# Kernel tuning notes

Measured on AMD Instinct MI355X. Metric: run time of the kernel, lower is better.

## Reference

```python
import jax, jax.numpy as jnp
import numpy as np

IN, HID, RANK, B = 2048, 2048, 512, 8192


def setup_inputs() -> dict:
    key = jax.random.key(0)
    ks = jax.random.split(key, 16)
    s_in = 1.0 / np.sqrt(IN + HID)
    s_r = 1.0 / np.sqrt(RANK)
    inp = {
        "x": jax.random.normal(ks[0], (B, IN), jnp.float32),
        "h": jax.random.normal(ks[1], (B, HID), jnp.float32),
        "c": jax.random.normal(ks[2], (B, HID), jnp.float32),
    }
    names = ["i", "f", "c", "o"]
    for idx, g in enumerate(names):
        inp[f"U{g}"] = jax.random.uniform(ks[3 + 3 * idx], (IN + HID, RANK), jnp.float32, -s_in, s_in)
        inp[f"V{g}"] = jax.random.uniform(ks[4 + 3 * idx], (RANK, HID), jnp.float32, -s_r, s_r)
        inp[f"b{g}"] = jnp.zeros((HID,), jnp.float32)
    return inp


def reference(x, h, c, Ui, Vi, bi, Uf, Vf, bf, Uc, Vc, bc, Uo, Vo, bo):
    combined = jnp.concatenate([x, h], axis=1)  # [B, IN+HID]

    def gate(U, V, b):
        return (combined @ U) @ V + b  # low-rank: [B,R] then [B,HID]

    i = jax.nn.sigmoid(gate(Ui, Vi, bi))
    f = jax.nn.sigmoid(gate(Uf, Vf, bf))
    o = jax.nn.sigmoid(gate(Uo, Vo, bo))
    c_hat = jnp.tanh(gate(Uc, Vc, bc))
    c_new = f * c + i * c_hat
    h_new = o * jnp.tanh(c_new)
    return (h_new, c_new)
```

## Files before the change

### kernel.cpp

```cpp
#include <hip/hip_runtime.h>
#include <hip/hip_bf16.h>
#include <cstdint>
#include <cstddef>

typedef __bf16 bf16;
typedef __bf16 bf16x8 __attribute__((ext_vector_type(8)));
typedef float f32x4 __attribute__((ext_vector_type(4)));

#define BATCH 8192
#define IN_DIM 2048
#define HID 2048
#define RANK 512
#define KDIM 4096
#define NG 2048
#define CHUNK_ROWS 4096


__device__ __forceinline__ void gload16(const void* g, void* l) {
  __builtin_amdgcn_global_load_lds(
      (const __attribute__((address_space(1))) unsigned int*)g,
      (__attribute__((address_space(3))) unsigned int*)l, 16, 0, 0);
}

__device__ __forceinline__ float sigmoidf_(float x) {
  return 1.0f / (1.0f + __expf(-x));
}
__device__ __forceinline__ float tanhf_(float x) {
  return 1.0f - 2.0f / (__expf(2.0f * x) + 1.0f);
}

#define GBAR  __builtin_amdgcn_s_barrier()
#define VMC4  asm volatile("s_waitcnt vmcnt(4)" ::: "memory")
#define VMC8  asm volatile("s_waitcnt vmcnt(8)" ::: "memory")
#define SB0   __builtin_amdgcn_sched_barrier(0)
#define LGKMC(N) do { asm volatile("s_waitcnt lgkmcnt(" #N ")" ::: "memory"); SB0; } while (0)

__device__ __forceinline__ void stage_half(const bf16* __restrict__ g0, int ld,
                                           int row0, int kcol, bf16* lbase, int tid) {
  const int wid = tid >> 6;
  #pragma unroll
  for (int q = 0; q < 2; ++q) {
    const int slot = q * 512 + tid;
    const int row = slot >> 3, cb = slot & 7;
    const int gcb = cb ^ (row & 7);
    gload16(g0 + (size_t)(row0 + row) * ld + kcol + gcb * 8,
            lbase + (size_t)(q * 64 + wid * 8) * 64);
  }
}

#define LD_APAR(PA, Q, P)                                                      \
  _Pragma("unroll") for (int ai = 0; ai < 2; ++ai)                             \
  _Pragma("unroll") for (int ks = 0; ks < 2; ++ks)                             \
    a[P][ai][ks] = *(const bf16x8*)((PA) + (wm + (Q) * 32 + ai * 16 + lr) * 64 \
                                 + ((((ks << 2) | lk) ^ sw) << 3));

#define LD_Bp(PB)                                                              \
  _Pragma("unroll") for (int j = 0; j < 4; ++j)                                \
  _Pragma("unroll") for (int ks = 0; ks < 2; ++ks)                             \
    b[j][ks] = *(const bf16x8*)((PB) + (wn + j * 16 + lr) * 64                 \
                                 + ((((ks << 2) | lk) ^ sw) << 3));

#define MFMAQP(Q, P)                                                           \
  _Pragma("unroll") for (int ai = 0; ai < 2; ++ai)                             \
  _Pragma("unroll") for (int ks = 0; ks < 2; ++ks)                             \
  _Pragma("unroll") for (int j = 0; j < 4; ++j)                                \
    acc[(Q) * 2 + ai][j] = __builtin_amdgcn_mfma_f32_16x16x32_bf16(            \
        a[P][ai][ks], b[j][ks], acc[(Q) * 2 + ai][j], 0, 0, 0);


template <int NT>
__device__ __forceinline__ void gemm_core(const bf16* __restrict__ A, int lda, int m0,
                                          const bf16* __restrict__ B, int ldb, int n0,
                                          bf16* lds, f32x4 (&acc)[8][4]) {
  const int tid = threadIdx.x;
  const int wid = tid >> 6, lane = tid & 63;
  const int wm = (wid >> 2) * 128, wn = (wid & 3) * 64;
  const int lr = lane & 15, lk = lane >> 4;
  const int sw = lr & 7;
  bf16x8 a[2][2][2];
  bf16x8 b[4][2];

  bf16* Ab0 = lds;
  bf16* Ab1 = lds + 16384;
  bf16* Rg0 = lds + 2 * 16384;
  bf16* Rg1 = lds + 3 * 16384;
  bf16* Rg2 = lds + 4 * 16384;

  #pragma unroll
  for (int i = 0; i < 8; ++i)
    #pragma unroll
    for (int j = 0; j < 4; ++j) acc[i][j] = (f32x4){0.f, 0.f, 0.f, 0.f};

  stage_half(A, lda, m0,       0,   Ab0,        tid);
  stage_half(A, lda, m0 + 128, 0,   Ab0 + 8192, tid);
  stage_half(B, ldb, n0,       0,   Rg0,        tid);
  stage_half(B, ldb, n0 + 128, 0,   Rg0 + 8192, tid);
  stage_half(B, ldb, n0,       64,  Rg1,        tid);
  stage_half(B, ldb, n0 + 128, 64,  Rg1 + 8192, tid);
  stage_half(B, ldb, n0,       128, Rg2,        tid);
  stage_half(B, ldb, n0 + 128, 128, Rg2 + 8192, tid);
  VMC8;
  GBAR;
  LD_Bp(Rg0);
  SB0;

  bf16 *pBc = Rg0, *pBn = Rg1, *pBn2 = Rg2;
  bf16 *pAc = Ab0, *pAa = Ab1;
  for (int c = 0; c < NT; ++c) {
    const int kc1 = ((c + 1) & (NT - 1)) * 64;
    const int kc3 = ((c + 3) & (NT - 1)) * 64;
    LD_APAR(pAc, 0, 0); LD_APAR(pAc, 1, 1); SB0;
    stage_half(A, lda, m0,       kc1, pAa,        tid); SB0;
    GBAR;
    LGKMC(4);
    __builtin_amdgcn_s_setprio(1); MFMAQP(0, 0); __builtin_amdgcn_s_setprio(0);
    LD_APAR(pAc, 2, 0); SB0;
    stage_half(A, lda, m0 + 128, kc1, pAa + 8192, tid); SB0;
    GBAR;
    LGKMC(4);
    __builtin_amdgcn_s_setprio(1); MFMAQP(1, 1); __builtin_amdgcn_s_setprio(0);
    LD_APAR(pAc, 3, 1); SB0;
    stage_half(B, ldb, n0,       kc3, pBc,        tid); SB0;
    GBAR;
    LGKMC(4);
    __builtin_amdgcn_s_setprio(1); MFMAQP(2, 0); __builtin_amdgcn_s_setprio(0);
    stage_half(B, ldb, n0 + 128, kc3, pBc + 8192, tid); SB0;
    VMC4;
    GBAR;
    LGKMC(0);
    __builtin_amdgcn_s_setprio(1); MFMAQP(3, 1); __builtin_amdgcn_s_setprio(0);
    LD_Bp(pBn);
    SB0;
    bf16* tt = pBc; pBc = pBn; pBn = pBn2; pBn2 = tt;
    tt = pAc; pAc = pAa; pAa = tt;
  }
}


__global__ void k_convert_combined(const float* __restrict__ x,
                                   const float* __restrict__ h,
                                   bf16* __restrict__ out) {
  size_t i4 = (size_t)blockIdx.x * blockDim.x + threadIdx.x;
  size_t base = i4 * 4;
  int col = (int)(base & (KDIM - 1));
  size_t row = base >> 12;
  const float* src = (col < IN_DIM) ? (x + row * IN_DIM + col)
                                    : (h + row * (size_t)HID + (col - IN_DIM));
  float4 v = *(const float4*)src;
  union { bf16 b[4]; uint2 u; } p;
  p.b[0] = (bf16)v.x; p.b[1] = (bf16)v.y; p.b[2] = (bf16)v.z; p.b[3] = (bf16)v.w;
  *(uint2*)(out + base) = p.u;
}


__global__ void k_tconv4(const float* __restrict__ s0, const float* __restrict__ s1,
                         const float* __restrict__ s2, const float* __restrict__ s3,
                         bf16* __restrict__ out, int nrow, int ncol,
                         long ostride, long gstride) {
  __shared__ float t[32][33];
  const float* in = blockIdx.z == 0 ? s0 : blockIdx.z == 1 ? s1
                  : blockIdx.z == 2 ? s2 : s3;
  bf16* o = out + (size_t)blockIdx.z * gstride;
  int c0 = blockIdx.x * 32, r0 = blockIdx.y * 32;
  int tx = threadIdx.x, ty = threadIdx.y;
  #pragma unroll
  for (int yy = ty; yy < 32; yy += 8)
    t[yy][tx] = in[(size_t)(r0 + yy) * ncol + c0 + tx];
  __syncthreads();
  #pragma unroll
  for (int yy = ty; yy < 32; yy += 8)
    o[(size_t)(c0 + yy) * ostride + r0 + tx] = (bf16)t[tx][yy];
}


__launch_bounds__(512, 2)
__global__ void k_gemm1(const bf16* __restrict__ A,
                        const bf16* __restrict__ Bt,
                        bf16* __restrict__ R) {
  __shared__ __align__(16) bf16 lds[81920];
  const int bx = blockIdx.x;
  const int id = (bx & 7) * 32 + (bx >> 3);
  const int m0 = (id >> 3) * 256, n0 = (id & 7) * 256;
  f32x4 acc[8][4];
  gemm_core<KDIM / 64>(A, KDIM, m0, Bt, KDIM, n0, lds, acc);

  const int tid = threadIdx.x;
  const int wid = tid >> 6, lane = tid & 63;
  const int wm = (wid >> 2) * 128, wn = (wid & 3) * 64;
  const int lr = lane & 15, lk = lane >> 4;
  #pragma unroll
  for (int i = 0; i < 8; ++i)
    #pragma unroll
    for (int j = 0; j < 4; ++j)
      #pragma unroll
      for (int v = 0; v < 4; ++v)
        R[(size_t)(m0 + wm + i * 16 + lk * 4 + v) * NG + (n0 + wn + j * 16 + lr)] =
            (bf16)acc[i][j][v];
}


__launch_bounds__(512, 2)
__global__ void k_gates(const bf16* __restrict__ Rb,
                        const bf16* __restrict__ Vt,
                        const float* __restrict__ b0, const float* __restrict__ b1,
                        const float* __restrict__ b2, const float* __restrict__ b3,
                        bf16* __restrict__ G, int m_base) {
  __shared__ __align__(16) bf16 lds[81920];
  const int bx = blockIdx.x;
  const int id = (bx & 7) * 64 + (bx >> 3);
  const int gate = id >> 7;
  const int mo = ((id >> 3) & 15) * 256;
  const int n0 = (id & 7) * 256;
  f32x4 acc[8][4];
  gemm_core<RANK / 64>(Rb + gate * RANK, NG, m_base + mo,
                       Vt + (size_t)gate * HID * RANK, RANK, n0, lds, acc);

  const int tid = threadIdx.x;
  const int wid = tid >> 6, lane = tid & 63;
  const int wm = (wid >> 2) * 128, wn = (wid & 3) * 64;
  const int lr = lane & 15, lk = lane >> 4;
  const float* bias = gate == 0 ? b0 : gate == 1 ? b1 : gate == 2 ? b2 : b3;
  const bool is_tanh = (gate == 2);
  bf16* Gg = G + (size_t)gate * CHUNK_ROWS * HID;
  #pragma unroll
  for (int j = 0; j < 4; ++j) {
    const int col = n0 + wn + j * 16 + lr;
    const float bj = bias[col];
    #pragma unroll
    for (int i = 0; i < 8; ++i)
      #pragma unroll
      for (int v = 0; v < 4; ++v) {
        const int row = mo + wm + i * 16 + lk * 4 + v;
        float p = acc[i][j][v] + bj;
        float av = is_tanh ? tanhf_(p) : sigmoidf_(p);
        Gg[(size_t)row * HID + col] = (bf16)av;
      }
  }
}


__global__ void k_ew(const bf16* __restrict__ G,
                     const float* __restrict__ cin,
                     float* __restrict__ hout, float* __restrict__ cout,
                     int m_base) {
  const size_t CHUNK = (size_t)CHUNK_ROWS * HID;
  const bf16* Gi = G;
  const bf16* Gf = G + CHUNK;
  const bf16* Gc = G + 2 * CHUNK;
  const bf16* Go = G + 3 * CHUNK;
  const size_t n8 = CHUNK / 8;
  for (size_t t = (size_t)blockIdx.x * blockDim.x + threadIdx.x; t < n8;
       t += (size_t)gridDim.x * blockDim.x) {
    size_t e = t * 8;
    bf16x8 vi = *(const bf16x8*)(Gi + e);
    bf16x8 vf = *(const bf16x8*)(Gf + e);
    bf16x8 vc = *(const bf16x8*)(Gc + e);
    bf16x8 vo = *(const bf16x8*)(Go + e);
    size_t ge = (size_t)m_base * HID + e;
    float4 c0 = *(const float4*)(cin + ge);
    float4 c1 = *(const float4*)(cin + ge + 4);
    float cc[8] = {c0.x, c0.y, c0.z, c0.w, c1.x, c1.y, c1.z, c1.w};
    float cn[8], hn[8];
    #pragma unroll
    for (int v = 0; v < 8; ++v) {
      float iv = (float)vi[v], fv = (float)vf[v], cv = (float)vc[v], ov = (float)vo[v];
      cn[v] = fv * cc[v] + iv * cv;
      hn[v] = ov * tanhf_(cn[v]);
    }
    *(float4*)(cout + ge)     = (float4){cn[0], cn[1], cn[2], cn[3]};
    *(float4*)(cout + ge + 4) = (float4){cn[4], cn[5], cn[6], cn[7]};
    *(float4*)(hout + ge)     = (float4){hn[0], hn[1], hn[2], hn[3]};
    *(float4*)(hout + ge + 4) = (float4){hn[4], hn[5], hn[6], hn[7]};
  }
}


extern "C" void kernel_launch(void* const* d_in, const int* in_sizes, int n_in,
                              void* d_out, int out_size, void* d_ws, size_t ws_size,
                              hipStream_t stream) {
  const float* x = (const float*)d_in[0];
  const float* h = (const float*)d_in[1];
  const float* c = (const float*)d_in[2];
  const float* U[4] = {(const float*)d_in[3], (const float*)d_in[6],
                       (const float*)d_in[9], (const float*)d_in[12]};
  const float* V[4] = {(const float*)d_in[4], (const float*)d_in[7],
                       (const float*)d_in[10], (const float*)d_in[13]};
  const float* b[4] = {(const float*)d_in[5], (const float*)d_in[8],
                       (const float*)d_in[11], (const float*)d_in[14]};

  char* ws = (char*)d_ws;
  bf16* combined = (bf16*)ws;
  bf16* Ut       = (bf16*)(ws + 67108864);
  bf16* Vt       = (bf16*)(ws + 67108864 + 16777216);
  bf16* Rbuf     = (bf16*)(ws + 67108864 + 16777216 + 8388608);
  bf16* G        = (bf16*)ws;

  float* hout = (float*)d_out;
  float* cout = hout + (size_t)BATCH * HID;

  k_convert_combined<<<(BATCH * (size_t)KDIM / 4) / 256, 256, 0, stream>>>(x, h, combined);

  k_tconv4<<<dim3(RANK / 32, KDIM / 32, 4), dim3(32, 8), 0, stream>>>(
      U[0], U[1], U[2], U[3], Ut, KDIM, RANK, KDIM, (long)RANK * KDIM);
  k_tconv4<<<dim3(HID / 32, RANK / 32, 4), dim3(32, 8), 0, stream>>>(
      V[0], V[1], V[2], V[3], Vt, RANK, HID, RANK, (long)HID * RANK);

  k_gemm1<<<256, 512, 0, stream>>>(combined, Ut, Rbuf);

  for (int chunk = 0; chunk < 2; ++chunk) {
    int m_base = chunk * CHUNK_ROWS;
    k_gates<<<512, 512, 0, stream>>>(Rbuf, Vt, b[0], b[1], b[2], b[3], G, m_base);
    k_ew<<<2048, 256, 0, stream>>>(G, c, hout, cout, m_base);
  }
}
```

Measured before the change: 343.6 us.

## Fuse gate GEMMs pairwise with elementwise LSTM cell update epilogues

Replaces the per-chunk gate GEMM plus separate elementwise kernel with two kernels. Each computes two gates' second-stage GEMMs on a 256x128 tile: the first writes sigmoid(i)*tanh(c_hat) as bf16, the second computes f and o and finishes c_new and h_new in its epilogue. This removes the four bf16 gate buffers and their round trip through memory. In exchange it uses a new smaller-tile GEMM core with a different wait schedule, holds two accumulator sets per thread (more register pressure), and the final epilogue does scalar, less coalesced fp32 loads and stores.

```diff
diff --git a/kernel.cpp b/kernel.cpp
--- a/kernel.cpp
+++ b/kernel.cpp
@@ -13,7 +13,6 @@
 #define RANK 512
 #define KDIM 4096
 #define NG 2048
-#define CHUNK_ROWS 4096
 
 
 __device__ __forceinline__ void gload16(const void* g, void* l) {
@@ -30,6 +29,8 @@
 }
 
 #define GBAR  __builtin_amdgcn_s_barrier()
+#define VMC0  asm volatile("s_waitcnt vmcnt(0)" ::: "memory")
+#define VMC2  asm volatile("s_waitcnt vmcnt(2)" ::: "memory")
 #define VMC4  asm volatile("s_waitcnt vmcnt(4)" ::: "memory")
 #define VMC8  asm volatile("s_waitcnt vmcnt(8)" ::: "memory")
 #define SB0   __builtin_amdgcn_sched_barrier(0)
@@ -48,16 +49,17 @@
   }
 }
 
+#define LD_Bp(PB)                                                              \
+  _Pragma("unroll") for (int j = 0; j < 4; ++j)                                \
+  _Pragma("unroll") for (int ks = 0; ks < 2; ++ks)                             \
+    b[j][ks] = *(const bf16x8*)((PB) + (wn + j * 16 + lr) * 64                 \
+                                 + ((((ks << 2) | lk) ^ sw) << 3));
+
+
 #define LD_APAR(PA, Q, P)                                                      \
   _Pragma("unroll") for (int ai = 0; ai < 2; ++ai)                             \
   _Pragma("unroll") for (int ks = 0; ks < 2; ++ks)                             \
     a[P][ai][ks] = *(const bf16x8*)((PA) + (wm + (Q) * 32 + ai * 16 + lr) * 64 \
-                                 + ((((ks << 2) | lk) ^ sw) << 3));
-
-#define LD_Bp(PB)                                                              \
-  _Pragma("unroll") for (int j = 0; j < 4; ++j)                                \
-  _Pragma("unroll") for (int ks = 0; ks < 2; ++ks)                             \
-    b[j][ks] = *(const bf16x8*)((PB) + (wn + j * 16 + lr) * 64                 \
                                  + ((((ks << 2) | lk) ^ sw) << 3));
 
 #define MFMAQP(Q, P)                                                           \
@@ -66,7 +68,6 @@
   _Pragma("unroll") for (int j = 0; j < 4; ++j)                                \
     acc[(Q) * 2 + ai][j] = __builtin_amdgcn_mfma_f32_16x16x32_bf16(            \
         a[P][ai][ks], b[j][ks], acc[(Q) * 2 + ai][j], 0, 0, 0);
-
 
 template <int NT>
 __device__ __forceinline__ void gemm_core(const bf16* __restrict__ A, int lda, int m0,
@@ -129,6 +130,81 @@
     GBAR;
     LGKMC(0);
     __builtin_amdgcn_s_setprio(1); MFMAQP(3, 1); __builtin_amdgcn_s_setprio(0);
+    LD_Bp(pBn);
+    SB0;
+    bf16* tt = pBc; pBc = pBn; pBn = pBn2; pBn2 = tt;
+    tt = pAc; pAc = pAa; pAa = tt;
+  }
+}
+
+
+#define LD_AP(PA, Q, P)                                                        \
+  _Pragma("unroll") for (int ks = 0; ks < 2; ++ks)                             \
+    ap[P][ks] = *(const bf16x8*)((PA) + (wm + (Q) * 16 + lr) * 64              \
+                                 + ((((ks << 2) | lk) ^ sw) << 3));
+
+#define MFMAP(Q, P)                                                            \
+  _Pragma("unroll") for (int ks = 0; ks < 2; ++ks)                             \
+  _Pragma("unroll") for (int j = 0; j < 4; ++j)                                \
+    acc[(Q)][j] = __builtin_amdgcn_mfma_f32_16x16x32_bf16(                     \
+        ap[P][ks], b[j][ks], acc[(Q)][j], 0, 0, 0);
+
+template <int NT>
+__device__ __forceinline__ void gemm_coreP(const bf16* __restrict__ A, int lda, int m0,
+                                           const bf16* __restrict__ B, int ldb, int n0,
+                                           bf16* lds, f32x4 (&acc)[4][4]) {
+  const int tid = threadIdx.x;
+  const int wid = tid >> 6, lane = tid & 63;
+  const int wm = (wid >> 1) * 64, wn = (wid & 1) * 64;
+  const int lr = lane & 15, lk = lane >> 4;
+  const int sw = lr & 7;
+  bf16x8 ap[2][2], b[4][2];
+
+  bf16* Ab0 = lds;
+  bf16* Ab1 = lds + 16384;
+  bf16* Rg0 = lds + 32768;
+  bf16* Rg1 = lds + 40960;
+  bf16* Rg2 = lds + 49152;
+
+  #pragma unroll
+  for (int i = 0; i < 4; ++i)
+    #pragma unroll
+    for (int j = 0; j < 4; ++j) acc[i][j] = (f32x4){0.f, 0.f, 0.f, 0.f};
+
+  stage_half(A, lda, m0,       0,   Ab0,        tid);
+  stage_half(A, lda, m0 + 128, 0,   Ab0 + 8192, tid);
+  stage_half(B, ldb, n0, 0,   Rg0, tid);
+  stage_half(B, ldb, n0, 64,  Rg1, tid);
+  stage_half(B, ldb, n0, 128, Rg2, tid);
+  VMC4;
+  GBAR;
+  LD_Bp(Rg0);
+  SB0;
+
+  bf16 *pBc = Rg0, *pBn = Rg1, *pBn2 = Rg2;
+  bf16 *pAc = Ab0, *pAa = Ab1;
+  for (int c = 0; c < NT; ++c) {
+    const int kc1 = ((c + 1) & (NT - 1)) * 64;
+    const int kc3 = ((c + 3) & (NT - 1)) * 64;
+    LD_AP(pAc, 0, 0); LD_AP(pAc, 1, 1); SB0;
+    stage_half(A, lda, m0,       kc1, pAa,        tid); SB0;
+    GBAR;
+    LGKMC(2);
+    __builtin_amdgcn_s_setprio(1); MFMAP(0, 0); __builtin_amdgcn_s_setprio(0);
+    LD_AP(pAc, 2, 0); SB0;
+    stage_half(A, lda, m0 + 128, kc1, pAa + 8192, tid); SB0;
+    GBAR;
+    LGKMC(2);
+    __builtin_amdgcn_s_setprio(1); MFMAP(1, 1); __builtin_amdgcn_s_setprio(0);
+    LD_AP(pAc, 3, 1); SB0;
+    stage_half(B, ldb, n0, kc3, pBc, tid); SB0;
+    GBAR;
+    LGKMC(2);
+    __builtin_amdgcn_s_setprio(1); MFMAP(2, 0); __builtin_amdgcn_s_setprio(0);
+    VMC2;
+    LGKMC(0);
+    GBAR;
+    __builtin_amdgcn_s_setprio(1); MFMAP(3, 1); __builtin_amdgcn_s_setprio(0);
     LD_Bp(pBn);
     SB0;
     bf16* tt = pBc; pBc = pBn; pBn = pBn2; pBn2 = tt;
@@ -200,77 +276,82 @@
 
 
 __launch_bounds__(512, 2)
-__global__ void k_gates(const bf16* __restrict__ Rb,
-                        const bf16* __restrict__ Vt,
-                        const float* __restrict__ b0, const float* __restrict__ b1,
-                        const float* __restrict__ b2, const float* __restrict__ b3,
-                        bf16* __restrict__ G, int m_base) {
-  __shared__ __align__(16) bf16 lds[81920];
+__global__ void k_pair_ic(const bf16* __restrict__ Rb,
+                          const bf16* __restrict__ Vt,
+                          const float* __restrict__ bi, const float* __restrict__ bc,
+                          bf16* __restrict__ sv) {
+  __shared__ __align__(16) bf16 lds[57344];
   const int bx = blockIdx.x;
   const int id = (bx & 7) * 64 + (bx >> 3);
-  const int gate = id >> 7;
-  const int mo = ((id >> 3) & 15) * 256;
-  const int n0 = (id & 7) * 256;
-  f32x4 acc[8][4];
-  gemm_core<RANK / 64>(Rb + gate * RANK, NG, m_base + mo,
-                       Vt + (size_t)gate * HID * RANK, RANK, n0, lds, acc);
-
-  const int tid = threadIdx.x;
-  const int wid = tid >> 6, lane = tid & 63;
-  const int wm = (wid >> 2) * 128, wn = (wid & 3) * 64;
-  const int lr = lane & 15, lk = lane >> 4;
-  const float* bias = gate == 0 ? b0 : gate == 1 ? b1 : gate == 2 ? b2 : b3;
-  const bool is_tanh = (gate == 2);
-  bf16* Gg = G + (size_t)gate * CHUNK_ROWS * HID;
+  const int m0 = (id >> 4) * 256, n0 = (id & 15) * 128;
+
+  f32x4 accI[4][4], accC[4][4];
+  gemm_coreP<RANK / 64>(Rb + 0 * RANK, NG, m0,
+                        Vt + (size_t)0 * HID * RANK, RANK, n0, lds, accI);
+  VMC0;
+  GBAR;
+  gemm_coreP<RANK / 64>(Rb + 2 * RANK, NG, m0,
+                        Vt + (size_t)2 * HID * RANK, RANK, n0, lds, accC);
+
+  const int tid = threadIdx.x;
+  const int wid = tid >> 6, lane = tid & 63;
+  const int wm = (wid >> 1) * 64, wn = (wid & 1) * 64;
+  const int lr = lane & 15, lk = lane >> 4;
   #pragma unroll
   for (int j = 0; j < 4; ++j) {
     const int col = n0 + wn + j * 16 + lr;
-    const float bj = bias[col];
-    #pragma unroll
-    for (int i = 0; i < 8; ++i)
+    const float bji = bi[col], bjc = bc[col];
+    #pragma unroll
+    for (int q = 0; q < 4; ++q)
       #pragma unroll
       for (int v = 0; v < 4; ++v) {
-        const int row = mo + wm + i * 16 + lk * 4 + v;
-        float p = acc[i][j][v] + bj;
-        float av = is_tanh ? tanhf_(p) : sigmoidf_(p);
-        Gg[(size_t)row * HID + col] = (bf16)av;
+        const int row = m0 + wm + q * 16 + lk * 4 + v;
+        const float s = sigmoidf_(accI[q][j][v] + bji) * tanhf_(accC[q][j][v] + bjc);
+        sv[(size_t)row * HID + col] = (bf16)s;
       }
   }
 }
 
 
-__global__ void k_ew(const bf16* __restrict__ G,
-                     const float* __restrict__ cin,
-                     float* __restrict__ hout, float* __restrict__ cout,
-                     int m_base) {
-  const size_t CHUNK = (size_t)CHUNK_ROWS * HID;
-  const bf16* Gi = G;
-  const bf16* Gf = G + CHUNK;
-  const bf16* Gc = G + 2 * CHUNK;
-  const bf16* Go = G + 3 * CHUNK;
-  const size_t n8 = CHUNK / 8;
-  for (size_t t = (size_t)blockIdx.x * blockDim.x + threadIdx.x; t < n8;
-       t += (size_t)gridDim.x * blockDim.x) {
-    size_t e = t * 8;
-    bf16x8 vi = *(const bf16x8*)(Gi + e);
-    bf16x8 vf = *(const bf16x8*)(Gf + e);
-    bf16x8 vc = *(const bf16x8*)(Gc + e);
-    bf16x8 vo = *(const bf16x8*)(Go + e);
-    size_t ge = (size_t)m_base * HID + e;
-    float4 c0 = *(const float4*)(cin + ge);
-    float4 c1 = *(const float4*)(cin + ge + 4);
-    float cc[8] = {c0.x, c0.y, c0.z, c0.w, c1.x, c1.y, c1.z, c1.w};
-    float cn[8], hn[8];
-    #pragma unroll
-    for (int v = 0; v < 8; ++v) {
-      float iv = (float)vi[v], fv = (float)vf[v], cv = (float)vc[v], ov = (float)vo[v];
-      cn[v] = fv * cc[v] + iv * cv;
-      hn[v] = ov * tanhf_(cn[v]);
-    }
-    *(float4*)(cout + ge)     = (float4){cn[0], cn[1], cn[2], cn[3]};
-    *(float4*)(cout + ge + 4) = (float4){cn[4], cn[5], cn[6], cn[7]};
-    *(float4*)(hout + ge)     = (float4){hn[0], hn[1], hn[2], hn[3]};
-    *(float4*)(hout + ge + 4) = (float4){hn[4], hn[5], hn[6], hn[7]};
+__launch_bounds__(512, 2)
+__global__ void k_pair_fo(const bf16* __restrict__ Rb,
+                          const bf16* __restrict__ Vt,
+                          const float* __restrict__ bf_, const float* __restrict__ bo,
+                          const bf16* __restrict__ sv,
+                          const float* __restrict__ cin,
+                          float* __restrict__ hout, float* __restrict__ cout) {
+  __shared__ __align__(16) bf16 lds[57344];
+  const int bx = blockIdx.x;
+  const int id = (bx & 7) * 64 + (bx >> 3);
+  const int m0 = (id >> 4) * 256, n0 = (id & 15) * 128;
+
+  f32x4 accF[4][4], accO[4][4];
+  gemm_coreP<RANK / 64>(Rb + 1 * RANK, NG, m0,
+                        Vt + (size_t)1 * HID * RANK, RANK, n0, lds, accF);
+  VMC0;
+  GBAR;
+  gemm_coreP<RANK / 64>(Rb + 3 * RANK, NG, m0,
+                        Vt + (size_t)3 * HID * RANK, RANK, n0, lds, accO);
+
+  const int tid = threadIdx.x;
+  const int wid = tid >> 6, lane = tid & 63;
+  const int wm = (wid >> 1) * 64, wn = (wid & 1) * 64;
+  const int lr = lane & 15, lk = lane >> 4;
+  #pragma unroll
+  for (int j = 0; j < 4; ++j) {
+    const int col = n0 + wn + j * 16 + lr;
+    const float bjf = bf_[col], bjo = bo[col];
+    #pragma unroll
+    for (int q = 0; q < 4; ++q)
+      #pragma unroll
+      for (int v = 0; v < 4; ++v) {
+        const int row = m0 + wm + q * 16 + lk * 4 + v;
+        const size_t e = (size_t)row * HID + col;
+        const float f = sigmoidf_(accF[q][j][v] + bjf);
+        const float cn = f * cin[e] + (float)sv[e];
+        cout[e] = cn;
+        hout[e] = sigmoidf_(accO[q][j][v] + bjo) * tanhf_(cn);
+      }
   }
 }
 
@@ -293,7 +374,7 @@
   bf16* Ut       = (bf16*)(ws + 67108864);
   bf16* Vt       = (bf16*)(ws + 67108864 + 16777216);
   bf16* Rbuf     = (bf16*)(ws + 67108864 + 16777216 + 8388608);
-  bf16* G        = (bf16*)ws;
+  bf16* sv       = (bf16*)ws;
 
   float* hout = (float*)d_out;
   float* cout = hout + (size_t)BATCH * HID;
@@ -307,9 +388,6 @@
 
   k_gemm1<<<256, 512, 0, stream>>>(combined, Ut, Rbuf);
 
-  for (int chunk = 0; chunk < 2; ++chunk) {
-    int m_base = chunk * CHUNK_ROWS;
-    k_gates<<<512, 512, 0, stream>>>(Rbuf, Vt, b[0], b[1], b[2], b[3], G, m_base);
-    k_ew<<<2048, 256, 0, stream>>>(G, c, hout, cout, m_base);
-  }
-}
+  k_pair_ic<<<512, 512, 0, stream>>>(Rbuf, Vt, b[0], b[2], sv);
+  k_pair_fo<<<512, 512, 0, stream>>>(Rbuf, Vt, b[1], b[3], sv, c, hout, cout);
+}
```

Result: faster. 332.3 us (-3.3%).
